# Performance work log

Hardware: AMD Instinct MI355X
Metric: run time of the kernel (lower is better)

## Reference

```python
import jax, jax.numpy as jnp
import numpy as np

B, S, D, H = 4, 2048, 1024, 16
HD = D // H
EPS = 1e-5


def setup_inputs() -> dict:
    key = jax.random.key(0)
    ks = jax.random.split(key, 12)
    scale = 1.0 / np.sqrt(D)
    inp = {
        "x": jax.random.normal(ks[0], (B, S, D), dtype=jnp.float32),
        "template_ids": jax.random.randint(ks[1], (B, S), 0, 1000, dtype=jnp.int64)
            if jax.config.jax_enable_x64 else jax.random.randint(ks[1], (B, S), 0, 1000, dtype=jnp.int32),
        "attention_mask": jnp.ones((B, S), dtype=jnp.int32),
        "Wq": jax.random.normal(ks[2], (D, D), dtype=jnp.float32) * scale,
        "bq": jnp.zeros((D,), dtype=jnp.float32),
        "Wk": jax.random.normal(ks[3], (D, D), dtype=jnp.float32) * scale,
        "bk": jnp.zeros((D,), dtype=jnp.float32),
        "Wv": jax.random.normal(ks[4], (D, D), dtype=jnp.float32) * scale,
        "bv": jnp.zeros((D,), dtype=jnp.float32),
        "Wo": jax.random.normal(ks[5], (D, D), dtype=jnp.float32) * scale,
        "bo": jnp.zeros((D,), dtype=jnp.float32),
        "gamma": jnp.ones((D,), dtype=jnp.float32),
        "beta": jnp.zeros((D,), dtype=jnp.float32),
    }
    return inp


def _split_heads(t):
    # [B,S,D] -> [B,H,S,HD]
    return t.reshape(B, S, H, HD).transpose(0, 2, 1, 3)


def reference(x, template_ids, attention_mask, Wq, bq, Wk, bk, Wv, bv, Wo, bo, gamma, beta):
    q = _split_heads(x @ Wq.T + bq)
    k = _split_heads(x @ Wk.T + bk)
    v = _split_heads(x @ Wv.T + bv)
    # [B,H,S,S]
    scores = jnp.einsum("bhqd,bhkd->bhqk", q, k) / jnp.sqrt(jnp.float32(HD))
    mask = attention_mask[:, None, None, :]  # broadcast over heads and query dim
    scores = jnp.where(mask == 0, jnp.float32(-10000.0), scores)
    attn = jax.nn.softmax(scores, axis=-1)  # dropout is identity in eval
    out = jnp.einsum("bhqk,bhkd->bhqd", attn, v)
    out = out.transpose(0, 2, 1, 3).reshape(B, S, D)
    out = out @ Wo.T + bo
    # residual + LayerNorm
    y = x + out
    mu = jnp.mean(y, axis=-1, keepdims=True)
    var = jnp.var(y, axis=-1, keepdims=True)
    return (y - mu) * jax.lax.rsqrt(var + EPS) * gamma + beta
```

## Files before the change

### kernel.cpp

```cpp
#include <hip/hip_runtime.h>

typedef unsigned short u16;
typedef unsigned int u32;
typedef __attribute__((ext_vector_type(8))) short bf16x8;
typedef __attribute__((ext_vector_type(4))) float f32x4;

#define NB 4
#define SS 2048
#define DD 1024
#define NH 16
#define HD 64
#define MM (NB*SS)

struct __align__(16) Pack16 { unsigned int w0, w1, w2, w3; };
union PU { Pack16 p; u16 s[8]; };

__device__ __forceinline__ float b2f(u16 u) {
    union { unsigned int i; float f; } v; v.i = ((unsigned int)u) << 16; return v.f;
}
__device__ __forceinline__ u16 f2b(float f) {
    union { unsigned int i; float f; } v; v.f = f;
    return (u16)((v.i + 0x7FFFu + ((v.i >> 16) & 1u)) >> 16);
}
__device__ __forceinline__ u32 packbf(float a, float b) {
    u32 ia = __float_as_uint(a), ib = __float_as_uint(b);
    return ((ia + 0x8000u) >> 16) | ((ib + 0x8000u) & 0xFFFF0000u);
}
__device__ __forceinline__ float rdS(const void* p, size_t i, int mode) {
    return mode ? ((const float*)p)[i] : b2f(((const u16*)p)[i]);
}
__device__ __forceinline__ float ex2(float x) { return __builtin_amdgcn_exp2f(x); }

__device__ __forceinline__ void cp16(const u16* g, u16* l) {
    __builtin_amdgcn_global_load_lds(
        (const __attribute__((address_space(1))) void*)g,
        (__attribute__((address_space(3))) void*)l, 16, 0, 0);
}

#define QSC 0.1803368801111204f
#define GX ((size_t)MM * DD / 8)
#define GW ((size_t)DD * DD / 8)
#define GTOT (GX + 4 * GW + 512)

__global__ __launch_bounds__(256) void convert_kernel(
    const void* __restrict__ x,
    const void* __restrict__ Wq, const void* __restrict__ Wk,
    const void* __restrict__ Wv, const void* __restrict__ Wo,
    const void* __restrict__ bq, const void* __restrict__ bk,
    const void* __restrict__ bv, const void* __restrict__ bo,
    u16* __restrict__ xb, u16* __restrict__ Wc, u16* __restrict__ Wob,
    u16* __restrict__ bcat, const u32* __restrict__ gamma_w)
{
    const int mode = (gamma_w[0] == 0x3F800000u) ? 1 : 0;
    size_t g = (size_t)blockIdx.x * 256 + threadIdx.x;
    const void* src; u16* dst; size_t off; float sc = 1.0f;
    if (g < GX)               { src = x;  dst = xb;              off = g * 8; }
    else if (g < GX + GW)     { src = Wq; dst = Wc;              off = (g - GX) * 8; sc = QSC; }
    else if (g < GX + 2 * GW) { src = Wk; dst = Wc + (size_t)DD * DD;     off = (g - GX - GW) * 8; }
    else if (g < GX + 3 * GW) { src = Wv; dst = Wc + (size_t)2 * DD * DD; off = (g - GX - 2 * GW) * 8; }
    else if (g < GX + 4 * GW) { src = Wo; dst = Wob;             off = (g - GX - 3 * GW) * 8; }
    else {
        size_t gg = g - (GX + 4 * GW);
        int which = (int)(gg >> 7); off = (gg & 127) * 8;
        src = (which == 0) ? bq : (which == 1) ? bk : (which == 2) ? bv : bo;
        dst = bcat + which * DD;
        if (which == 0) sc = QSC;
    }
    PU o;
    if (mode) {
        const float* s = (const float*)src + off;
        float4 a = ((const float4*)s)[0];
        float4 b = ((const float4*)s)[1];
        o.s[0] = f2b(a.x * sc); o.s[1] = f2b(a.y * sc);
        o.s[2] = f2b(a.z * sc); o.s[3] = f2b(a.w * sc);
        o.s[4] = f2b(b.x * sc); o.s[5] = f2b(b.y * sc);
        o.s[6] = f2b(b.z * sc); o.s[7] = f2b(b.w * sc);
    } else {
        PU in; in.p = *(const Pack16*)((const u16*)src + off);
#pragma unroll
        for (int j = 0; j < 8; j++) o.s[j] = f2b(b2f(in.s[j]) * sc);
    }
    *(Pack16*)(dst + off) = o.p;
}

__global__ __launch_bounds__(256) void gemm_qkv(
    const u16* __restrict__ xb, const u16* __restrict__ Wc, const u16* __restrict__ bcat,
    u16* __restrict__ Q, u16* __restrict__ K, u16* __restrict__ V)
{
    __shared__ __align__(16) u16 sh[2 * 128 * 64];
    u16* As = sh;
    u16* Bs = sh + 128 * 64;

    const int tid  = threadIdx.x;
    const int wv   = tid >> 6;
    const int lane = tid & 63;
    const int wy = wv >> 1, wx = wv & 1;
    const int l15 = lane & 15, quad = lane >> 4;
    const int m0 = blockIdx.x * 128, n0 = blockIdx.y * 128;
    const int srow = lane >> 3;
    const int sw   = ((lane & 7) ^ srow) * 8;
    const int key  = l15 & 7;

    f32x4 acc[4][4];
#pragma unroll
    for (int i = 0; i < 4; i++)
#pragma unroll
        for (int j = 0; j < 4; j++) acc[i][j] = (f32x4){0.f, 0.f, 0.f, 0.f};

    for (int k0 = 0; k0 < DD; k0 += 64) {
#pragma unroll
        for (int c = 0; c < 4; c++) {
            cp16(&xb[(size_t)(m0 + wv * 32 + c * 8 + srow) * DD + k0 + sw],
                 &As[wv * 2048 + c * 512]);
            cp16(&Wc[(size_t)(n0 + wv * 32 + c * 8 + srow) * DD + k0 + sw],
                 &Bs[wv * 2048 + c * 512]);
        }
        __syncthreads();
#pragma unroll
        for (int ks = 0; ks < 2; ks++) {
            bf16x8 a[4], bb[4];
#pragma unroll
            for (int mt = 0; mt < 4; mt++)
                a[mt] = *(const bf16x8*)&As[(wy * 64 + mt * 16 + l15) * 64 +
                                            (((ks << 2) + quad) ^ key) * 8];
#pragma unroll
            for (int nt = 0; nt < 4; nt++)
                bb[nt] = *(const bf16x8*)&Bs[(wx * 64 + nt * 16 + l15) * 64 +
                                             (((ks << 2) + quad) ^ key) * 8];
#pragma unroll
            for (int mt = 0; mt < 4; mt++)
#pragma unroll
                for (int nt = 0; nt < 4; nt++)
                    acc[mt][nt] = __builtin_amdgcn_mfma_f32_16x16x32_bf16(
                        a[mt], bb[nt], acc[mt][nt], 0, 0, 0);
        }
        __syncthreads();
    }

    const int z = n0 >> 10;
    if (z != 2) {
        u16* out = (z == 0) ? Q : K;
#pragma unroll
        for (int nt = 0; nt < 4; nt++) {
            int n_g = n0 + wx * 64 + nt * 16 + l15;
            float bv_ = b2f(bcat[n_g]);
            int nn = n_g & 1023;
            int h = nn >> 6, hd = nn & 63;
#pragma unroll
            for (int mt = 0; mt < 4; mt++) {
#pragma unroll
                for (int r = 0; r < 4; r++) {
                    int m_g = m0 + wy * 64 + mt * 16 + quad * 4 + r;
                    int b = m_g >> 11, s = m_g & (SS - 1);
                    out[(((size_t)(b * NH + h) * SS) + s) * HD + hd] =
                        f2b(acc[mt][nt][r] + bv_);
                }
            }
        }
    } else {
        const int bb_ = m0 >> 11, sbase = m0 & (SS - 1);
#pragma unroll
        for (int ph = 0; ph < 2; ph++) {
            if (wx == ph) {
#pragma unroll
                for (int nt = 0; nt < 4; nt++) {
                    int n_loc = nt * 16 + l15;
                    float bv_ = b2f(bcat[n0 + ph * 64 + n_loc]);
#pragma unroll
                    for (int mt = 0; mt < 4; mt++) {
                        int m = wy * 64 + mt * 16 + quad * 4;
                        uint2 wr;
                        wr.x = (u32)f2b(acc[mt][nt][0] + bv_) |
                               ((u32)f2b(acc[mt][nt][1] + bv_) << 16);
                        wr.y = (u32)f2b(acc[mt][nt][2] + bv_) |
                               ((u32)f2b(acc[mt][nt][3] + bv_) << 16);
                        *(uint2*)&sh[n_loc * 136 + m] = wr;
                    }
                }
            }
            __syncthreads();
            {
                int row = tid >> 2;
                int sg  = tid & 3;
                int n_g = n0 + ph * 64 + row;
                int nn = n_g & 1023;
                int h = nn >> 6, hd = nn & 63;
                u16* dst = &V[(((size_t)(bb_ * NH + h)) * HD + hd) * SS + sbase];
#pragma unroll
                for (int j = 0; j < 4; j++) {
                    int mloc = sg * 32 + j * 8;
                    *(Pack16*)&dst[mloc] = *(const Pack16*)&sh[row * 136 + mloc];
                }
            }
            __syncthreads();
        }
    }
}

__global__ __launch_bounds__(256, 3) void attn_kernel(
    const u16* __restrict__ Q, const u16* __restrict__ K, const u16* __restrict__ V,
    const int* __restrict__ mask, u16* __restrict__ O)
{
    const int bh = blockIdx.y;
    const int b = bh >> 4, h = bh & 15;
    const int q0 = blockIdx.x * 128;
    const u16* Qp  = Q + (size_t)bh * SS * HD;
    const u16* Kp  = K + (size_t)bh * SS * HD;
    const u16* Vtg = V + (size_t)bh * HD * SS;
    const int* mk = mask + b * SS;

    __shared__ __align__(16) u16 Kl[2 * 64 * 64];
    __shared__ __align__(16) u16 Vt[2 * 64 * 64];
    __shared__ __align__(16) u16 Pw[4 * 32 * 72];
    __shared__ int s_anymask;

    const int tid  = threadIdx.x;
    const int w    = tid >> 6;
    const int lane = tid & 63;
    const int l15 = lane & 15, quad = lane >> 4;
    const int srow = lane >> 3;
    const int sw   = ((lane & 7) ^ srow) * 8;
    const int key  = l15 & 7;
    u16* Pme = &Pw[w * 2304];

    if (tid == 0) s_anymask = 0;
    __syncthreads();
    {
        int local = 0;
#pragma unroll
        for (int i = 0; i < 2; i++) {
            int4 m4 = ((const int4*)mk)[i * 256 + tid];
            if ((m4.x == 0) | (m4.y == 0) | (m4.z == 0) | (m4.w == 0)) local = 1;
        }
        if (local) s_anymask = 1;
    }
    __syncthreads();
    const bool anymask = (s_anymask != 0);

    bf16x8 qf[2][2];
#pragma unroll
    for (int qt = 0; qt < 2; qt++)
#pragma unroll
        for (int ks = 0; ks < 2; ks++)
            qf[qt][ks] = *(const bf16x8*)&Qp[(size_t)(q0 + w * 32 + qt * 16 + l15) * HD +
                                             ks * 32 + quad * 8];

    f32x4 oacc[2][4];
#pragma unroll
    for (int i = 0; i < 2; i++)
#pragma unroll
        for (int j = 0; j < 4; j++) oacc[i][j] = (f32x4){0.f, 0.f, 0.f, 0.f};

    float lsum[2] = {0.f, 0.f};

#pragma unroll
    for (int c = 0; c < 2; c++) {
        cp16(&Kp[(size_t)(w * 16 + c * 8 + srow) * HD + sw], &Kl[w * 1024 + c * 512]);
        cp16(&Vtg[(size_t)(w * 16 + c * 8 + srow) * SS + sw], &Vt[w * 1024 + c * 512]);
    }

    for (int it = 0; it < SS / 64; it++) {
        const int kv0 = it * 64;
        const int p = it & 1;
        __syncthreads();

        if (it + 1 < SS / 64) {
            const int kn = kv0 + 64;
#pragma unroll
            for (int c = 0; c < 2; c++) {
                cp16(&Kp[(size_t)(kn + w * 16 + c * 8 + srow) * HD + sw],
                     &Kl[(p ^ 1) * 4096 + w * 1024 + c * 512]);
                cp16(&Vtg[(size_t)(w * 16 + c * 8 + srow) * SS + kn + sw],
                     &Vt[(p ^ 1) * 4096 + w * 1024 + c * 512]);
            }
        }

        f32x4 sacc[4][2];
#pragma unroll
        for (int i = 0; i < 4; i++)
#pragma unroll
            for (int j = 0; j < 2; j++) sacc[i][j] = (f32x4){0.f, 0.f, 0.f, 0.f};
#pragma unroll
        for (int ks = 0; ks < 2; ks++) {
            bf16x8 kf[4];
#pragma unroll
            for (int kvt = 0; kvt < 4; kvt++)
                kf[kvt] = *(const bf16x8*)&Kl[p * 4096 + (kvt * 16 + l15) * 64 +
                                              (((ks << 2) + quad) ^ key) * 8];
#pragma unroll
            for (int kvt = 0; kvt < 4; kvt++)
#pragma unroll
                for (int qt = 0; qt < 2; qt++)
                    sacc[kvt][qt] = __builtin_amdgcn_mfma_f32_16x16x32_bf16(
                        kf[kvt], qf[qt][ks], sacc[kvt][qt], 0, 0, 0);
        }

#pragma unroll
        for (int kvt = 0; kvt < 4; kvt++)
#pragma unroll
            for (int qt = 0; qt < 2; qt++) {
                f32x4 vv = sacc[kvt][qt];
                if (anymask) {
#pragma unroll
                    for (int r = 0; r < 4; r++) {
                        int kv = kv0 + kvt * 16 + quad * 4 + r;
                        if (mk[kv] == 0) vv[r] = -20000.0f;
                    }
                }
                float p0 = ex2(vv[0]);
                float p1 = ex2(vv[1]);
                float p2 = ex2(vv[2]);
                float p3 = ex2(vv[3]);
                lsum[qt] += (p0 + p1) + (p2 + p3);
                uint2 wr; wr.x = packbf(p0, p1); wr.y = packbf(p2, p3);
                *(uint2*)&Pme[(qt * 16 + l15) * 72 + kvt * 16 + quad * 4] = wr;
            }

#pragma unroll
        for (int ks2 = 0; ks2 < 2; ks2++) {
            bf16x8 vf[4];
#pragma unroll
            for (int nt = 0; nt < 4; nt++)
                vf[nt] = *(const bf16x8*)&Vt[p * 4096 + (nt * 16 + l15) * 64 +
                                             (((ks2 << 2) + quad) ^ key) * 8];
#pragma unroll
            for (int qt = 0; qt < 2; qt++) {
                bf16x8 af = *(const bf16x8*)&Pme[(qt * 16 + l15) * 72 +
                                                 ks2 * 32 + quad * 8];
#pragma unroll
                for (int nt = 0; nt < 4; nt++)
                    oacc[qt][nt] = __builtin_amdgcn_mfma_f32_16x16x32_bf16(
                        af, vf[nt], oacc[qt][nt], 0, 0, 0);
            }
        }
    }

#pragma unroll
    for (int qt = 0; qt < 2; qt++) {
        lsum[qt] += __shfl_xor(lsum[qt], 16, 64);
        lsum[qt] += __shfl_xor(lsum[qt], 32, 64);
    }
#pragma unroll
    for (int qt = 0; qt < 2; qt++) {
#pragma unroll
        for (int r = 0; r < 4; r++) {
            float inv = 1.0f / __shfl(lsum[qt], quad * 4 + r, 64);
            int row = q0 + w * 32 + qt * 16 + quad * 4 + r;
            size_t base = ((size_t)(b * SS + row)) * DD + h * HD;
#pragma unroll
            for (int nt = 0; nt < 4; nt++)
                O[base + nt * 16 + l15] = f2b(oacc[qt][nt][r] * inv);
        }
    }
}

__global__ __launch_bounds__(256) void gemm_oproj(
    const u16* __restrict__ A, const u16* __restrict__ Wob, const u16* __restrict__ bcat,
    u16* __restrict__ Y)
{
    __shared__ __align__(16) u16 As[128 * 64];
    __shared__ __align__(16) u16 Bs[128 * 64];

    const int tid  = threadIdx.x;
    const int wv   = tid >> 6;
    const int lane = tid & 63;
    const int wy = wv >> 1, wx = wv & 1;
    const int l15 = lane & 15, quad = lane >> 4;
    const int m0 = blockIdx.x * 128, n0 = blockIdx.y * 128;
    const int srow = lane >> 3;
    const int sw   = ((lane & 7) ^ srow) * 8;
    const int key  = l15 & 7;

    f32x4 acc[4][4];
#pragma unroll
    for (int i = 0; i < 4; i++)
#pragma unroll
        for (int j = 0; j < 4; j++) acc[i][j] = (f32x4){0.f, 0.f, 0.f, 0.f};

    for (int k0 = 0; k0 < DD; k0 += 64) {
#pragma unroll
        for (int c = 0; c < 4; c++) {
            cp16(&A[(size_t)(m0 + wv * 32 + c * 8 + srow) * DD + k0 + sw],
                 &As[wv * 2048 + c * 512]);
            cp16(&Wob[(size_t)(n0 + wv * 32 + c * 8 + srow) * DD + k0 + sw],
                 &Bs[wv * 2048 + c * 512]);
        }
        __syncthreads();
#pragma unroll
        for (int ks = 0; ks < 2; ks++) {
            bf16x8 a[4], bb[4];
#pragma unroll
            for (int mt = 0; mt < 4; mt++)
                a[mt] = *(const bf16x8*)&As[(wy * 64 + mt * 16 + l15) * 64 +
                                            (((ks << 2) + quad) ^ key) * 8];
#pragma unroll
            for (int nt = 0; nt < 4; nt++)
                bb[nt] = *(const bf16x8*)&Bs[(wx * 64 + nt * 16 + l15) * 64 +
                                             (((ks << 2) + quad) ^ key) * 8];
#pragma unroll
            for (int mt = 0; mt < 4; mt++)
#pragma unroll
                for (int nt = 0; nt < 4; nt++)
                    acc[mt][nt] = __builtin_amdgcn_mfma_f32_16x16x32_bf16(
                        a[mt], bb[nt], acc[mt][nt], 0, 0, 0);
        }
        __syncthreads();
    }

#pragma unroll
    for (int nt = 0; nt < 4; nt++) {
        int n_g = n0 + wx * 64 + nt * 16 + l15;
        float bv_ = b2f(bcat[3 * DD + n_g]);
#pragma unroll
        for (int mt = 0; mt < 4; mt++) {
#pragma unroll
            for (int r = 0; r < 4; r++) {
                int m_g = m0 + wy * 64 + mt * 16 + quad * 4 + r;
                Y[(size_t)m_g * DD + n_g] = f2b(acc[mt][nt][r] + bv_);
            }
        }
    }
}

__global__ __launch_bounds__(256) void ln_kernel(
    const u16* __restrict__ Yp, const void* __restrict__ x,
    const void* __restrict__ gamma, const void* __restrict__ beta,
    void* __restrict__ out)
{
    const int mode = (((const u32*)gamma)[0] == 0x3F800000u) ? 1 : 0;
    const int w    = threadIdx.x >> 6;
    const int lane = threadIdx.x & 63;
    const int row  = blockIdx.x * 4 + w;
    const u16* y = Yp + (size_t)row * DD;

    float vals[16];
    float s = 0.f, sq = 0.f;
#pragma unroll
    for (int i = 0; i < 2; i++) {
        PU d; d.p = *(const Pack16*)&y[i * 512 + lane * 8];
        if (mode) {
            const float* xp = (const float*)x + (size_t)row * DD + i * 512 + lane * 8;
            float4 xa = ((const float4*)xp)[0];
            float4 xb2 = ((const float4*)xp)[1];
            float xr[8] = {xa.x, xa.y, xa.z, xa.w, xb2.x, xb2.y, xb2.z, xb2.w};
#pragma unroll
            for (int j = 0; j < 8; j++) {
                float f = b2f(d.s[j]) + xr[j];
                vals[i * 8 + j] = f;
                s += f; sq += f * f;
            }
        } else {
            const u16* xp = (const u16*)x + (size_t)row * DD + i * 512 + lane * 8;
            PU xd; xd.p = *(const Pack16*)xp;
#pragma unroll
            for (int j = 0; j < 8; j++) {
                float f = b2f(d.s[j]) + b2f(xd.s[j]);
                vals[i * 8 + j] = f;
                s += f; sq += f * f;
            }
        }
    }
#pragma unroll
    for (int off = 1; off < 64; off <<= 1) {
        s  += __shfl_xor(s, off);
        sq += __shfl_xor(sq, off);
    }
    float mu  = s * (1.0f / 1024.0f);
    float var = sq * (1.0f / 1024.0f) - mu * mu;
    float rs  = rsqrtf(var + 1e-5f);

#pragma unroll
    for (int i = 0; i < 2; i++) {
        float r8[8];
#pragma unroll
        for (int j = 0; j < 8; j++) {
            int col = i * 512 + lane * 8 + j;
            r8[j] = (vals[i * 8 + j] - mu) * rs * rdS(gamma, col, mode) + rdS(beta, col, mode);
        }
        if (mode) {
            float* of = (float*)out + (size_t)row * DD + i * 512 + lane * 8;
            ((float4*)of)[0] = make_float4(r8[0], r8[1], r8[2], r8[3]);
            ((float4*)of)[1] = make_float4(r8[4], r8[5], r8[6], r8[7]);
        } else {
            PU ob;
#pragma unroll
            for (int j = 0; j < 8; j++) ob.s[j] = f2b(r8[j]);
            *(Pack16*)((u16*)out + (size_t)row * DD + i * 512 + lane * 8) = ob.p;
        }
    }
}

extern "C" void kernel_launch(void* const* d_in, const int* in_sizes, int n_in,
                              void* d_out, int out_size, void* d_ws, size_t ws_size,
                              hipStream_t stream)
{
    const void* x     = d_in[0];
    const int* mask   = (const int*)d_in[2];
    const void* Wq    = d_in[3];
    const void* bq    = d_in[4];
    const void* Wk    = d_in[5];
    const void* bk    = d_in[6];
    const void* Wv    = d_in[7];
    const void* bv    = d_in[8];
    const void* Wo    = d_in[9];
    const void* bo    = d_in[10];
    const void* gamma = d_in[11];
    const void* beta  = d_in[12];

    const size_t n = (size_t)MM * DD;
    u16* xb   = (u16*)((char*)d_ws + 256);
    u16* Wc   = xb + n;
    u16* Wob  = Wc + (size_t)3 * DD * DD;
    u16* bcat = Wob + (size_t)DD * DD;
    u16* Qb   = bcat + 4096;
    u16* Kb   = Qb + n;
    u16* Vb   = Kb + n;
    u16* Ab   = Vb + n;
    u16* Yb   = xb;

    convert_kernel<<<(unsigned)(GTOT / 256), 256, 0, stream>>>(
        x, Wq, Wk, Wv, Wo, bq, bk, bv, bo, xb, Wc, Wob, bcat, (const u32*)gamma);
    gemm_qkv<<<dim3(MM / 128, 3 * DD / 128), 256, 0, stream>>>(xb, Wc, bcat, Qb, Kb, Vb);
    attn_kernel<<<dim3(SS / 128, NB * NH), 256, 0, stream>>>(Qb, Kb, Vb, mask, Ab);
    gemm_oproj<<<dim3(MM / 128, DD / 128), 256, 0, stream>>>(Ab, Wob, bcat, Yb);
    ln_kernel<<<MM / 4, 256, 0, stream>>>(Yb, x, gamma, beta, d_out);
}
```

Measured before the change: 334.6 us.

## Keep attention probabilities in registers via permlane swaps instead of LDS

Replaces the per-warp LDS round-trip for the softmax probability tile with in-register repacking using v_permlane32_swap and v_permlane16_swap, so the MFMA A-operand is built directly from the S accumulators. This removes the P shared buffer, which lowers LDS use. With that smaller footprint, the launch-bounds occupancy hint rises from 3 to 4 blocks, and s_setprio is raised around the MFMA sections. Risks include a wrong lane permutation mapping and register pressure from the higher occupancy target.

New measurement: 327.5 us. 2.1% less time.

```diff
diff --git a/kernel.cpp b/kernel.cpp
--- a/kernel.cpp
+++ b/kernel.cpp
@@ -35,6 +35,13 @@
     __builtin_amdgcn_global_load_lds(
         (const __attribute__((address_space(1))) void*)g,
         (__attribute__((address_space(3))) void*)l, 16, 0, 0);
+}
+
+__device__ __forceinline__ void pl32swap(u32& a, u32& b) {
+    asm volatile("v_permlane32_swap_b32 %0, %1" : "+v"(a), "+v"(b));
+}
+__device__ __forceinline__ void pl16swap(u32& a, u32& b) {
+    asm volatile("v_permlane16_swap_b32 %0, %1" : "+v"(a), "+v"(b));
 }
 
 #define QSC 0.1803368801111204f
@@ -197,7 +204,7 @@
     }
 }
 
-__global__ __launch_bounds__(256, 3) void attn_kernel(
+__global__ __launch_bounds__(256, 4) void attn_kernel(
     const u16* __restrict__ Q, const u16* __restrict__ K, const u16* __restrict__ V,
     const int* __restrict__ mask, u16* __restrict__ O)
 {
@@ -211,7 +218,6 @@
 
     __shared__ __align__(16) u16 Kl[2 * 64 * 64];
     __shared__ __align__(16) u16 Vt[2 * 64 * 64];
-    __shared__ __align__(16) u16 Pw[4 * 32 * 72];
     __shared__ int s_anymask;
 
     const int tid  = threadIdx.x;
@@ -221,7 +227,6 @@
     const int srow = lane >> 3;
     const int sw   = ((lane & 7) ^ srow) * 8;
     const int key  = l15 & 7;
-    u16* Pme = &Pw[w * 2304];
 
     if (tid == 0) s_anymask = 0;
     __syncthreads();
@@ -287,18 +292,22 @@
             for (int kvt = 0; kvt < 4; kvt++)
                 kf[kvt] = *(const bf16x8*)&Kl[p * 4096 + (kvt * 16 + l15) * 64 +
                                               (((ks << 2) + quad) ^ key) * 8];
+            __builtin_amdgcn_s_setprio(1);
 #pragma unroll
             for (int kvt = 0; kvt < 4; kvt++)
 #pragma unroll
                 for (int qt = 0; qt < 2; qt++)
                     sacc[kvt][qt] = __builtin_amdgcn_mfma_f32_16x16x32_bf16(
                         kf[kvt], qf[qt][ks], sacc[kvt][qt], 0, 0, 0);
-        }
-
-#pragma unroll
-        for (int kvt = 0; kvt < 4; kvt++)
-#pragma unroll
-            for (int qt = 0; qt < 2; qt++) {
+            __builtin_amdgcn_s_setprio(0);
+        }
+
+        union { bf16x8 v; u32 d[4]; } paf[2][2];
+#pragma unroll
+        for (int qt = 0; qt < 2; qt++) {
+            u32 pk[4][2];
+#pragma unroll
+            for (int kvt = 0; kvt < 4; kvt++) {
                 f32x4 vv = sacc[kvt][qt];
                 if (anymask) {
 #pragma unroll
@@ -312,9 +321,22 @@
                 float p2 = ex2(vv[2]);
                 float p3 = ex2(vv[3]);
                 lsum[qt] += (p0 + p1) + (p2 + p3);
-                uint2 wr; wr.x = packbf(p0, p1); wr.y = packbf(p2, p3);
-                *(uint2*)&Pme[(qt * 16 + l15) * 72 + kvt * 16 + quad * 4] = wr;
-            }
+                pk[kvt][0] = packbf(p0, p1);
+                pk[kvt][1] = packbf(p2, p3);
+            }
+#pragma unroll
+            for (int ks2 = 0; ks2 < 2; ks2++) {
+#pragma unroll
+                for (int c = 0; c < 2; c++) {
+                    u32 x0 = pk[ks2 * 2 + 0][c];
+                    u32 x1 = pk[ks2 * 2 + 1][c];
+                    pl32swap(x0, x1);
+                    pl16swap(x0, x1);
+                    paf[qt][ks2].d[c]     = x0;
+                    paf[qt][ks2].d[2 + c] = x1;
+                }
+            }
+        }
 
 #pragma unroll
         for (int ks2 = 0; ks2 < 2; ks2++) {
@@ -323,15 +345,15 @@
             for (int nt = 0; nt < 4; nt++)
                 vf[nt] = *(const bf16x8*)&Vt[p * 4096 + (nt * 16 + l15) * 64 +
                                              (((ks2 << 2) + quad) ^ key) * 8];
+            __builtin_amdgcn_s_setprio(1);
 #pragma unroll
             for (int qt = 0; qt < 2; qt++) {
-                bf16x8 af = *(const bf16x8*)&Pme[(qt * 16 + l15) * 72 +
-                                                 ks2 * 32 + quad * 8];
 #pragma unroll
                 for (int nt = 0; nt < 4; nt++)
                     oacc[qt][nt] = __builtin_amdgcn_mfma_f32_16x16x32_bf16(
-                        af, vf[nt], oacc[qt][nt], 0, 0, 0);
-            }
+                        paf[qt][ks2].v, vf[nt], oacc[qt][nt], 0, 0, 0);
+            }
+            __builtin_amdgcn_s_setprio(0);
         }
     }
 
```
